# Kernel tuning notes

Hardware: AMD Instinct MI355X
Metric: run time of the kernel (lower is better)

## Reference

```python
import jax, jax.numpy as jnp
import numpy as np

B, S, D, H = 8, 2048, 1024, 16
A = D // H  # attn_dim = 64
SCALE = float(np.sqrt(D))  # module divides by sqrt(d_model), NOT sqrt(attn_dim)


def setup_inputs() -> dict:
    key = jax.random.key(0)
    ks = jax.random.split(key, 6)
    # xavier-uniform bound for Linear(dim -> attn_dim)
    bound = float(np.sqrt(6.0 / (D + A)))
    return {
        "query": jax.random.normal(ks[0], (B, S, D), dtype=jnp.float32),
        "key": jax.random.normal(ks[1], (B, S, D), dtype=jnp.float32),
        "value": jax.random.normal(ks[2], (B, S, D), dtype=jnp.float32),
        "Wq": jax.random.uniform(ks[3], (D, A), jnp.float32, -bound, bound),
        "bq": jnp.zeros((A,), jnp.float32),
        "Wk": jax.random.uniform(ks[4], (D, A), jnp.float32, -bound, bound),
        "bk": jnp.zeros((A,), jnp.float32),
        "Wv": jax.random.uniform(ks[5], (D, A), jnp.float32, -bound, bound),
        "bv": jnp.zeros((A,), jnp.float32),
    }


def reference(query, key, value, Wq, bq, Wk, bk, Wv, bv):
    # Linear projections dim -> attn_dim
    q = query @ Wq + bq  # [B, S, A]
    k = key @ Wk + bk    # [B, S, A]
    v = value @ Wv + bv  # [B, S, A]
    # scaled dot-product attention; score matrix [B, S, S] is materialized
    score = jnp.einsum("bqa,bka->bqk", q, k) / SCALE
    attn = jax.nn.softmax(score, axis=-1)
    # dropout is identity in eval mode
    context = jnp.einsum("bqk,bka->bqa", attn, v)  # [B, S, A]
    return (context, attn)
```

## Files before the change

kernel.cpp:

```cpp
#include <hip/hip_runtime.h>
#include <hip/hip_bf16.h>

#define NB 8
#define SEQ 2048
#define DM 1024
#define AD 64
#define NROWS (NB * SEQ)

#define SCL2 0.04508422f

typedef __attribute__((ext_vector_type(8))) short short8;
typedef __attribute__((ext_vector_type(4))) float f32x4;

static __device__ __forceinline__ unsigned short f2bf(float f) {
    unsigned int u = __float_as_uint(f);
    u += 0x7FFFu + ((u >> 16) & 1u);
    return (unsigned short)(u >> 16);
}

static __device__ __forceinline__ f32x4 mfma16(short8 a, short8 b, f32x4 c) {
    return __builtin_amdgcn_mfma_f32_16x16x32_bf16(a, b, c, 0, 0, 0);
}

static __device__ __forceinline__ short8 pack8v(f32x4 a, f32x4 b) {
    short8 r;
    r[0] = (short)f2bf(a[0]); r[1] = (short)f2bf(a[1]);
    r[2] = (short)f2bf(a[2]); r[3] = (short)f2bf(a[3]);
    r[4] = (short)f2bf(b[0]); r[5] = (short)f2bf(b[1]);
    r[6] = (short)f2bf(b[2]); r[7] = (short)f2bf(b[3]);
    return r;
}

__global__ __launch_bounds__(256) void wT_kernel(
    const float* __restrict__ Wq, const float* __restrict__ Wk,
    const float* __restrict__ Wv, unsigned short* __restrict__ wT) {
    int p = blockIdx.y;
    int k0 = blockIdx.x * 64;
    const float* W = (p == 0) ? Wq : (p == 1) ? Wk : Wv;
    __shared__ unsigned short tl[64][72];
    int t = threadIdx.x;
    int c = t & 63;
    int r0 = t >> 6;
    for (int i = 0; i < 16; i++) {
        int k = r0 + i * 4;
        tl[c][k] = f2bf(W[(size_t)(k0 + k) * AD + c]);
    }
    __syncthreads();
    for (int i = 0; i < 16; i++) {
        int a = r0 + i * 4;
        wT[((size_t)p * AD + a) * DM + k0 + c] = tl[a][c];
    }
}

__global__ __launch_bounds__(256, 2) void proj_kernel(
    const float* __restrict__ q_in, const float* __restrict__ k_in,
    const float* __restrict__ v_in, const float* __restrict__ bq,
    const float* __restrict__ bk, const float* __restrict__ bv,
    const unsigned short* __restrict__ wT,
    unsigned short* __restrict__ q_out, unsigned short* __restrict__ k_out,
    unsigned short* __restrict__ vT_out) {
    int p = blockIdx.y;
    int rbase = blockIdx.x * 64;
    const float* X = (p == 0) ? q_in : (p == 1) ? k_in : v_in;
    const float* bias = (p == 0) ? bq : (p == 1) ? bk : bv;
    const unsigned short* wTp = wT + (size_t)p * AD * DM;

    __shared__ float xs[2][64][68];
    __shared__ unsigned short wsm[2][64][72];

    int t = threadIdx.x;
    int lane = t & 63;
    int w = t >> 6;
    int arow = lane & 15;
    int agrp = lane >> 4;

    int srow = t >> 4;
    int scol = (t & 15) * 4;
    int wrow = t >> 2;
    int wcol = (t & 3) * 16;

    const float* Xb = X + (size_t)rbase * DM;

    f32x4 acc[4];
#pragma unroll
    for (int ct = 0; ct < 4; ct++) acc[ct] = (f32x4){0.f, 0.f, 0.f, 0.f};

    float4 px0, px1, px2, px3;
    float4 pw0, pw1;

    px0 = *reinterpret_cast<const float4*>(&Xb[(size_t)(0 * 16 + srow) * DM + scol]);
    px1 = *reinterpret_cast<const float4*>(&Xb[(size_t)(1 * 16 + srow) * DM + scol]);
    px2 = *reinterpret_cast<const float4*>(&Xb[(size_t)(2 * 16 + srow) * DM + scol]);
    px3 = *reinterpret_cast<const float4*>(&Xb[(size_t)(3 * 16 + srow) * DM + scol]);
    {
        const char* wp = reinterpret_cast<const char*>(wTp + (size_t)wrow * DM + wcol);
        pw0 = *reinterpret_cast<const float4*>(wp);
        pw1 = *reinterpret_cast<const float4*>(wp + 16);
    }
    *reinterpret_cast<float4*>(&xs[0][0 * 16 + srow][scol]) = px0;
    *reinterpret_cast<float4*>(&xs[0][1 * 16 + srow][scol]) = px1;
    *reinterpret_cast<float4*>(&xs[0][2 * 16 + srow][scol]) = px2;
    *reinterpret_cast<float4*>(&xs[0][3 * 16 + srow][scol]) = px3;
    *reinterpret_cast<float4*>(&wsm[0][wrow][wcol]) = pw0;
    *reinterpret_cast<float4*>(&wsm[0][wrow][wcol + 8]) = pw1;
    __syncthreads();

    for (int c = 0; c < 16; ++c) {
        int bu = c & 1;
        if (c < 15) {
            int kb = (c + 1) * 64;
            px0 = *reinterpret_cast<const float4*>(&Xb[(size_t)(0 * 16 + srow) * DM + kb + scol]);
            px1 = *reinterpret_cast<const float4*>(&Xb[(size_t)(1 * 16 + srow) * DM + kb + scol]);
            px2 = *reinterpret_cast<const float4*>(&Xb[(size_t)(2 * 16 + srow) * DM + kb + scol]);
            px3 = *reinterpret_cast<const float4*>(&Xb[(size_t)(3 * 16 + srow) * DM + kb + scol]);
            const char* wp = reinterpret_cast<const char*>(wTp + (size_t)wrow * DM + kb + wcol);
            pw0 = *reinterpret_cast<const float4*>(wp);
            pw1 = *reinterpret_cast<const float4*>(wp + 16);
        }
        const float* xr = &xs[bu][w * 16 + arow][0];
#pragma unroll
        for (int s = 0; s < 2; ++s) {
            f32x4 a0 = *reinterpret_cast<const f32x4*>(&xr[s * 32 + agrp * 8]);
            f32x4 a1 = *reinterpret_cast<const f32x4*>(&xr[s * 32 + agrp * 8 + 4]);
            short8 af = pack8v(a0, a1);
#pragma unroll
            for (int ct = 0; ct < 4; ++ct) {
                short8 bf = *reinterpret_cast<const short8*>(
                    &wsm[bu][ct * 16 + arow][s * 32 + agrp * 8]);
                acc[ct] = mfma16(af, bf, acc[ct]);
            }
        }
        if (c < 15) {
            int bo = bu ^ 1;
            *reinterpret_cast<float4*>(&xs[bo][0 * 16 + srow][scol]) = px0;
            *reinterpret_cast<float4*>(&xs[bo][1 * 16 + srow][scol]) = px1;
            *reinterpret_cast<float4*>(&xs[bo][2 * 16 + srow][scol]) = px2;
            *reinterpret_cast<float4*>(&xs[bo][3 * 16 + srow][scol]) = px3;
            *reinterpret_cast<float4*>(&wsm[bo][wrow][wcol]) = pw0;
            *reinterpret_cast<float4*>(&wsm[bo][wrow][wcol + 8]) = pw1;
        }
        __syncthreads();
    }

    if (p < 2) {
        unsigned short* outp = (p == 0) ? q_out : k_out;
#pragma unroll
        for (int ct = 0; ct < 4; ct++) {
            int a = ct * 16 + arow;
            float bv_ = bias[a];
#pragma unroll
            for (int rr = 0; rr < 4; rr++) {
                int row = rbase + w * 16 + agrp * 4 + rr;
                outp[(size_t)row * AD + a] = f2bf(acc[ct][rr] + bv_);
            }
        }
    } else {
        unsigned short* sc = (unsigned short*)&xs[0][0][0];
#pragma unroll
        for (int ct = 0; ct < 4; ct++) {
            int a = ct * 16 + arow;
            float bv_ = bias[a];
#pragma unroll
            for (int rr = 0; rr < 4; rr++) {
                int row = w * 16 + agrp * 4 + rr;
                sc[a * 72 + row] = f2bf(acc[ct][rr] + bv_);
            }
        }
        __syncthreads();
        int bidx = rbase >> 11;
        int sbase = rbase & 2047;
        int rr = t & 63;
        for (int i = 0; i < 16; i++) {
            int a = (t >> 6) + i * 4;
            vT_out[((size_t)bidx * AD + a) * SEQ + sbase + rr] = sc[a * 72 + rr];
        }
    }
}

__global__ __launch_bounds__(128, 6) void sum_kernel(
    const unsigned short* __restrict__ qb, const unsigned short* __restrict__ kb,
    float* __restrict__ rowsumpart) {
    int blk = blockIdx.x;
    int b = blk & 7;
    int sp = (blk >> 3) & 3;
    int qbase = (blk >> 5) * 32;

    __shared__ float wsum[2][32];

    int t = threadIdx.x;
    int lane = t & 63;
    int w = t >> 6;
    int arow = lane & 15;
    int agrp = lane >> 4;

    const unsigned short* qrow = qb + ((size_t)b * SEQ + qbase) * AD;
    short8 qf0a = *reinterpret_cast<const short8*>(qrow + (size_t)arow * AD + agrp * 8);
    short8 qf1a = *reinterpret_cast<const short8*>(qrow + (size_t)arow * AD + 32 + agrp * 8);
    short8 qf0b = *reinterpret_cast<const short8*>(qrow + (size_t)(16 + arow) * AD + agrp * 8);
    short8 qf1b = *reinterpret_cast<const short8*>(qrow + (size_t)(16 + arow) * AD + 32 + agrp * 8);
    const unsigned short* kbp = kb + (size_t)b * SEQ * AD;

    int keybase = sp * 512 + w * 256;
    float sA[4] = {0.f, 0.f, 0.f, 0.f};
    float sB[4] = {0.f, 0.f, 0.f, 0.f};
    for (int kt = 0; kt < 16; ++kt) {
        int key0 = keybase + kt * 16;
        const unsigned short* krow = kbp + (size_t)(key0 + arow) * AD;
        short8 kf0 = *reinterpret_cast<const short8*>(krow + agrp * 8);
        short8 kf1 = *reinterpret_cast<const short8*>(krow + 32 + agrp * 8);
        f32x4 aA = (f32x4){0.f, 0.f, 0.f, 0.f};
        aA = mfma16(qf0a, kf0, aA);
        aA = mfma16(qf1a, kf1, aA);
        f32x4 aB = (f32x4){0.f, 0.f, 0.f, 0.f};
        aB = mfma16(qf0b, kf0, aB);
        aB = mfma16(qf1b, kf1, aB);
#pragma unroll
        for (int r = 0; r < 4; r++) {
            sA[r] += __builtin_amdgcn_exp2f(aA[r] * SCL2);
            sB[r] += __builtin_amdgcn_exp2f(aB[r] * SCL2);
        }
    }
#pragma unroll
    for (int r = 0; r < 4; r++) {
#pragma unroll
        for (int off = 1; off < 16; off <<= 1) {
            sA[r] += __shfl_xor(sA[r], off);
            sB[r] += __shfl_xor(sB[r], off);
        }
    }
    if (arow == 0) {
#pragma unroll
        for (int r = 0; r < 4; r++) {
            wsum[w][agrp * 4 + r] = sA[r];
            wsum[w][16 + agrp * 4 + r] = sB[r];
        }
    }
    __syncthreads();
    if (t < 32)
        rowsumpart[(size_t)sp * NROWS + (size_t)b * SEQ + qbase + t] =
            wsum[0][t] + wsum[1][t];
}

__global__ __launch_bounds__(256) void lr_kernel(
    const float* __restrict__ part, float* __restrict__ lr_g) {
    int i = blockIdx.x * 256 + threadIdx.x;
    float S = part[i] + part[NROWS + i] + part[2 * NROWS + i] + part[3 * NROWS + i];
    lr_g[i] = -__builtin_amdgcn_logf(S);
}

__global__ __launch_bounds__(128, 3) void attn2_kernel(
    const unsigned short* __restrict__ qb, const unsigned short* __restrict__ kb,
    const unsigned short* __restrict__ vT, const float* __restrict__ lr_g,
    float* __restrict__ attn_out, float* __restrict__ ctxpart) {
    int blk = blockIdx.x;
    int b = blk & 7;
    int sp = (blk >> 3) & 3;
    int qbase = (blk >> 5) * 32;

    __shared__ float sf[2][32][68];
    __shared__ float lr_lds[32];

    int t = threadIdx.x;
    int lane = t & 63;
    int w = t >> 6;
    int arow = lane & 15;
    int agrp = lane >> 4;

    if (t < 32) lr_lds[t] = lr_g[(size_t)b * SEQ + qbase + t];

    const unsigned short* qrow = qb + ((size_t)b * SEQ + qbase) * AD;
    short8 qf0a = *reinterpret_cast<const short8*>(qrow + (size_t)arow * AD + agrp * 8);
    short8 qf1a = *reinterpret_cast<const short8*>(qrow + (size_t)arow * AD + 32 + agrp * 8);
    short8 qf0b = *reinterpret_cast<const short8*>(qrow + (size_t)(16 + arow) * AD + agrp * 8);
    short8 qf1b = *reinterpret_cast<const short8*>(qrow + (size_t)(16 + arow) * AD + 32 + agrp * 8);
    const unsigned short* kbp = kb + (size_t)b * SEQ * AD;
    const unsigned short* vTb = vT + (size_t)b * AD * SEQ;
    float* attn_b = attn_out + ((size_t)b * SEQ + qbase) * SEQ;
    __syncthreads();

    float lrA[4], lrB[4];
#pragma unroll
    for (int r = 0; r < 4; r++) {
        lrA[r] = lr_lds[agrp * 4 + r];
        lrB[r] = lr_lds[16 + agrp * 4 + r];
    }

    f32x4 caccA[4], caccB[4];
#pragma unroll
    for (int ct = 0; ct < 4; ct++) {
        caccA[ct] = (f32x4){0.f, 0.f, 0.f, 0.f};
        caccB[ct] = (f32x4){0.f, 0.f, 0.f, 0.f};
    }

    int keybase = sp * 512 + w * 256;
    for (int g = 0; g < 4; ++g) {
        int key0b = keybase + g * 64;
#pragma unroll
        for (int kb4 = 0; kb4 < 4; ++kb4) {
            int k0 = key0b + kb4 * 16;
            const unsigned short* krow = kbp + (size_t)(k0 + arow) * AD;
            short8 kf0 = *reinterpret_cast<const short8*>(krow + agrp * 8);
            short8 kf1 = *reinterpret_cast<const short8*>(krow + 32 + agrp * 8);
            f32x4 aA = (f32x4){0.f, 0.f, 0.f, 0.f};
            aA = mfma16(qf0a, kf0, aA);
            aA = mfma16(qf1a, kf1, aA);
            f32x4 aB = (f32x4){0.f, 0.f, 0.f, 0.f};
            aB = mfma16(qf0b, kf0, aB);
            aB = mfma16(qf1b, kf1, aB);
#pragma unroll
            for (int r = 0; r < 4; r++) {
                sf[w][agrp * 4 + r][kb4 * 16 + arow] =
                    __builtin_amdgcn_exp2f(aA[r] * SCL2 + lrA[r]);
                sf[w][16 + agrp * 4 + r][kb4 * 16 + arow] =
                    __builtin_amdgcn_exp2f(aB[r] * SCL2 + lrB[r]);
            }
        }
#pragma unroll
        for (int j = 0; j < 8; ++j) {
            int row = j * 4 + agrp;
            int c4 = arow * 4;
            f32x4 vv = *reinterpret_cast<const f32x4*>(&sf[w][row][c4]);
            __builtin_nontemporal_store(
                vv, reinterpret_cast<f32x4*>(&attn_b[(size_t)row * SEQ + key0b + c4]));
        }
#pragma unroll
        for (int ks = 0; ks < 2; ++ks) {
            f32x4 pa0 = *reinterpret_cast<const f32x4*>(&sf[w][arow][ks * 32 + agrp * 8]);
            f32x4 pa1 = *reinterpret_cast<const f32x4*>(&sf[w][arow][ks * 32 + agrp * 8 + 4]);
            short8 pfA = pack8v(pa0, pa1);
            f32x4 pb0 = *reinterpret_cast<const f32x4*>(&sf[w][16 + arow][ks * 32 + agrp * 8]);
            f32x4 pb1 = *reinterpret_cast<const f32x4*>(&sf[w][16 + arow][ks * 32 + agrp * 8 + 4]);
            short8 pfB = pack8v(pb0, pb1);
#pragma unroll
            for (int ct = 0; ct < 4; ct++) {
                const unsigned short* vr =
                    vTb + (size_t)(ct * 16 + arow) * SEQ + key0b + ks * 32 + agrp * 8;
                short8 vv = *reinterpret_cast<const short8*>(vr);
                caccA[ct] = mfma16(pfA, vv, caccA[ct]);
                caccB[ct] = mfma16(pfB, vv, caccB[ct]);
            }
        }
    }

    if (w == 1) {
#pragma unroll
        for (int ct = 0; ct < 4; ct++)
#pragma unroll
            for (int r = 0; r < 4; r++) {
                sf[1][agrp * 4 + r][ct * 16 + arow] = caccA[ct][r];
                sf[1][16 + agrp * 4 + r][ct * 16 + arow] = caccB[ct][r];
            }
    }
    __syncthreads();
    if (w == 0) {
        float* cp = ctxpart + (size_t)sp * NROWS * AD;
#pragma unroll
        for (int ct = 0; ct < 4; ct++)
#pragma unroll
            for (int r = 0; r < 4; r++) {
                float vA = caccA[ct][r] + sf[1][agrp * 4 + r][ct * 16 + arow];
                cp[((size_t)b * SEQ + qbase + agrp * 4 + r) * AD + ct * 16 + arow] = vA;
                float vB = caccB[ct][r] + sf[1][16 + agrp * 4 + r][ct * 16 + arow];
                cp[((size_t)b * SEQ + qbase + 16 + agrp * 4 + r) * AD + ct * 16 + arow] = vB;
            }
    }
}

__global__ __launch_bounds__(256) void ctx_kernel(
    const float* __restrict__ ctxpart, float* __restrict__ ctx_out) {
    int i4 = blockIdx.x * 256 + threadIdx.x;
    const f32x4* p = reinterpret_cast<const f32x4*>(ctxpart);
    const int plane = NROWS * AD / 4;
    f32x4 a = p[i4], b = p[plane + i4], c = p[2 * plane + i4], d = p[3 * plane + i4];
    f32x4 r = a + b + c + d;
    __builtin_nontemporal_store(r, reinterpret_cast<f32x4*>(ctx_out) + i4);
}

extern "C" void kernel_launch(void* const* d_in, const int* in_sizes, int n_in,
                              void* d_out, int out_size, void* d_ws, size_t ws_size,
                              hipStream_t stream) {
    const float* q_in = (const float*)d_in[0];
    const float* k_in = (const float*)d_in[1];
    const float* v_in = (const float*)d_in[2];
    const float* Wq = (const float*)d_in[3];
    const float* bq = (const float*)d_in[4];
    const float* Wk = (const float*)d_in[5];
    const float* bk = (const float*)d_in[6];
    const float* Wv = (const float*)d_in[7];
    const float* bv = (const float*)d_in[8];

    char* ws = (char*)d_ws;
    unsigned short* q_bf = (unsigned short*)(ws);
    unsigned short* k_bf = (unsigned short*)(ws + (2u << 20));
    unsigned short* vT   = (unsigned short*)(ws + (4u << 20));
    unsigned short* wT   = (unsigned short*)(ws + (6u << 20));
    float* rowsumpart    = (float*)(ws + (7u << 20));
    float* lr_g          = (float*)(ws + (7u << 20) + (256u << 10));
    float* ctxpart       = (float*)(ws + (8u << 20));

    float* ctx_out = (float*)d_out;
    float* attn_out = ctx_out + (size_t)NB * SEQ * AD;

    hipLaunchKernelGGL(wT_kernel, dim3(16, 3), dim3(256), 0, stream, Wq, Wk, Wv, wT);
    hipLaunchKernelGGL(proj_kernel, dim3(256, 3), dim3(256), 0, stream,
                       q_in, k_in, v_in, bq, bk, bv, wT, q_bf, k_bf, vT);
    hipLaunchKernelGGL(sum_kernel, dim3(2048), dim3(128), 0, stream,
                       q_bf, k_bf, rowsumpart);
    hipLaunchKernelGGL(lr_kernel, dim3(64), dim3(256), 0, stream, rowsumpart, lr_g);
    hipLaunchKernelGGL(attn2_kernel, dim3(2048), dim3(128), 0, stream,
                       q_bf, k_bf, vT, lr_g, attn_out, ctxpart);
    hipLaunchKernelGGL(ctx_kernel, dim3(1024), dim3(256), 0, stream, ctxpart, ctx_out);
}
```

Baseline: 112.4 us.

## Cover full key range per block with 8 waves, reduce context in LDS

The attention kernel now launches 512 blocks of 512 threads, so each block's 8 waves span all 2048 keys for a 32-query tile instead of splitting keys across 4 blocks. Partial context accumulators are reduced in shared memory and written straight to the output. This removes the ctxpart workspace round-trip and the separate ctx_kernel launch. In exchange, LDS use per block grows to about 70KB, which limits occupancy, and there are fewer blocks to fill the GPU.

```diff
diff --git a/kernel.cpp b/kernel.cpp
--- a/kernel.cpp
+++ b/kernel.cpp
@@ -248,16 +248,15 @@
     lr_g[i] = -__builtin_amdgcn_logf(S);
 }
 
-__global__ __launch_bounds__(128, 3) void attn2_kernel(
+__global__ __launch_bounds__(512, 2) void attn2_kernel(
     const unsigned short* __restrict__ qb, const unsigned short* __restrict__ kb,
     const unsigned short* __restrict__ vT, const float* __restrict__ lr_g,
-    float* __restrict__ attn_out, float* __restrict__ ctxpart) {
+    float* __restrict__ attn_out, float* __restrict__ ctx_out) {
     int blk = blockIdx.x;
     int b = blk & 7;
-    int sp = (blk >> 3) & 3;
-    int qbase = (blk >> 5) * 32;
-
-    __shared__ float sf[2][32][68];
+    int qbase = (blk >> 3) * 32;
+
+    __shared__ float sf[8][32][68];
     __shared__ float lr_lds[32];
 
     int t = threadIdx.x;
@@ -292,7 +291,7 @@
         caccB[ct] = (f32x4){0.f, 0.f, 0.f, 0.f};
     }
 
-    int keybase = sp * 512 + w * 256;
+    int keybase = w * 256;
     for (int g = 0; g < 4; ++g) {
         int key0b = keybase + g * 64;
 #pragma unroll
@@ -342,38 +341,23 @@
         }
     }
 
-    if (w == 1) {
-#pragma unroll
-        for (int ct = 0; ct < 4; ct++)
-#pragma unroll
-            for (int r = 0; r < 4; r++) {
-                sf[1][agrp * 4 + r][ct * 16 + arow] = caccA[ct][r];
-                sf[1][16 + agrp * 4 + r][ct * 16 + arow] = caccB[ct][r];
-            }
-    }
-    __syncthreads();
-    if (w == 0) {
-        float* cp = ctxpart + (size_t)sp * NROWS * AD;
-#pragma unroll
-        for (int ct = 0; ct < 4; ct++)
-#pragma unroll
-            for (int r = 0; r < 4; r++) {
-                float vA = caccA[ct][r] + sf[1][agrp * 4 + r][ct * 16 + arow];
-                cp[((size_t)b * SEQ + qbase + agrp * 4 + r) * AD + ct * 16 + arow] = vA;
-                float vB = caccB[ct][r] + sf[1][16 + agrp * 4 + r][ct * 16 + arow];
-                cp[((size_t)b * SEQ + qbase + 16 + agrp * 4 + r) * AD + ct * 16 + arow] = vB;
-            }
-    }
-}
-
-__global__ __launch_bounds__(256) void ctx_kernel(
-    const float* __restrict__ ctxpart, float* __restrict__ ctx_out) {
-    int i4 = blockIdx.x * 256 + threadIdx.x;
-    const f32x4* p = reinterpret_cast<const f32x4*>(ctxpart);
-    const int plane = NROWS * AD / 4;
-    f32x4 a = p[i4], b = p[plane + i4], c = p[2 * plane + i4], d = p[3 * plane + i4];
-    f32x4 r = a + b + c + d;
-    __builtin_nontemporal_store(r, reinterpret_cast<f32x4*>(ctx_out) + i4);
+    __syncthreads();
+#pragma unroll
+    for (int ct = 0; ct < 4; ct++)
+#pragma unroll
+        for (int r = 0; r < 4; r++) {
+            sf[w][agrp * 4 + r][ct * 16 + arow] = caccA[ct][r];
+            sf[w][16 + agrp * 4 + r][ct * 16 + arow] = caccB[ct][r];
+        }
+    __syncthreads();
+
+    float* ctx_b = ctx_out + ((size_t)b * SEQ + qbase) * AD;
+    for (int i = t; i < 32 * 64; i += 512) {
+        int r = i >> 6, a = i & 63;
+        float v = ((sf[0][r][a] + sf[1][r][a]) + (sf[2][r][a] + sf[3][r][a])) +
+                  ((sf[4][r][a] + sf[5][r][a]) + (sf[6][r][a] + sf[7][r][a]));
+        __builtin_nontemporal_store(v, &ctx_b[(size_t)r * AD + a]);
+    }
 }
 
 extern "C" void kernel_launch(void* const* d_in, const int* in_sizes, int n_in,
@@ -396,7 +380,6 @@
     unsigned short* wT   = (unsigned short*)(ws + (6u << 20));
     float* rowsumpart    = (float*)(ws + (7u << 20));
     float* lr_g          = (float*)(ws + (7u << 20) + (256u << 10));
-    float* ctxpart       = (float*)(ws + (8u << 20));
 
     float* ctx_out = (float*)d_out;
     float* attn_out = ctx_out + (size_t)NB * SEQ * AD;
@@ -407,7 +390,6 @@
     hipLaunchKernelGGL(sum_kernel, dim3(2048), dim3(128), 0, stream,
                        q_bf, k_bf, rowsumpart);
     hipLaunchKernelGGL(lr_kernel, dim3(64), dim3(256), 0, stream, rowsumpart, lr_g);
-    hipLaunchKernelGGL(attn2_kernel, dim3(2048), dim3(128), 0, stream,
-                       q_bf, k_bf, vT, lr_g, attn_out, ctxpart);
-    hipLaunchKernelGGL(ctx_kernel, dim3(1024), dim3(256), 0, stream, ctxpart, ctx_out);
-}
+    hipLaunchKernelGGL(attn2_kernel, dim3(512), dim3(512), 0, stream,
+                       q_bf, k_bf, vT, lr_g, attn_out, ctx_out);
+}
```

New measurement: 107.5 us. -4.4%, faster.
